# Optimization experiments

Hardware: AMD Instinct MI355X
Metric: run time of the kernel (lower is better)

## Reference

```python
import jax, jax.numpy as jnp
import numpy as np
from jax import lax

B_, S_, IN_, HID_ = 64, 512, 1024, 1024


def setup_inputs() -> dict:
    key = jax.random.key(0)
    k1, k2, k3, k4 = jax.random.split(key, 4)
    stdv = 1.0 / np.sqrt(HID_)
    return {
        "x": jax.random.normal(k1, (B_, S_, IN_), dtype=jnp.float32),
        "U": jax.random.uniform(k2, (IN_, 4 * HID_), minval=-stdv, maxval=stdv, dtype=jnp.float32),
        "V": jax.random.uniform(k3, (HID_, 4 * HID_), minval=-stdv, maxval=stdv, dtype=jnp.float32),
        "B": jax.random.uniform(k4, (4 * HID_,), minval=-stdv, maxval=stdv, dtype=jnp.float32),
        "h0": jnp.zeros((B_, HID_), dtype=jnp.float32),
        "c0": jnp.zeros((B_, HID_), dtype=jnp.float32),
    }


def reference(x, U, V, B, h0, c0):
    hd = h0.shape[-1]

    def step(carry, x_t):
        h, c = carry
        # [batch, 4*hid] combined gate pre-activation
        g = x_t @ U + h @ V + B
        n = jnp.tanh(g[:, 0:hd])                      # candidate (N_T)
        i = jax.nn.sigmoid(g[:, hd:2 * hd])           # input gate (I_T)
        f = jax.nn.sigmoid(g[:, 2 * hd:3 * hd])       # forget gate (F_T)
        o = jax.nn.sigmoid(g[:, 3 * hd:4 * hd])       # output gate (O_T)
        c_new = c * f + n * i                          # R_T
        h_new = jnp.tanh(c_new) * o                    # U_T
        return (h_new, c_new), h_new

    (h_fin, c_fin), ys = lax.scan(step, (h0, c0), jnp.swapaxes(x, 0, 1))
    out = jnp.swapaxes(ys, 0, 1)  # [batch, seq, hid]
    return out, (h_fin, c_fin)
```

## Files before the change

### kernel.cpp

```cpp
#include <hip/hip_runtime.h>
#include <stdint.h>


#define OUT_HF  33554432
#define OUT_CF  33619968

typedef __attribute__((ext_vector_type(8))) short bf16x8;
typedef __attribute__((ext_vector_type(4))) float f32x4;
typedef __attribute__((ext_vector_type(4))) unsigned short u16x4;
typedef __attribute__((ext_vector_type(4))) unsigned int u32x4;

#define WS_G    0
#define WS_XB   268435456
#define WS_HB   268435456
#define WS_UT   335544320

__device__ __forceinline__ unsigned short f2bf(float f) {
  unsigned u = __float_as_uint(f);
  u += 0x7FFFu + ((u >> 16) & 1u);
  return (unsigned short)(u >> 16);
}
__device__ __forceinline__ float bf2f(unsigned short b) {
  return __uint_as_float(((unsigned)b) << 16);
}
__device__ __forceinline__ float sigf(float x)   { return 1.0f / (1.0f + __expf(-x)); }
__device__ __forceinline__ float tanhf_(float x) { return 2.0f / (1.0f + __expf(-2.0f * x)) - 1.0f; }

__global__ void convert_x(const float* __restrict__ x, unsigned short* __restrict__ xb) {
  const int i = (blockIdx.x * 256 + threadIdx.x) * 4;
  f32x4 v = *(const f32x4*)(x + i);
  u16x4 o;
  o[0] = f2bf(v[0]); o[1] = f2bf(v[1]); o[2] = f2bf(v[2]); o[3] = f2bf(v[3]);
  *(u16x4*)(xb + i) = o;
}

__global__ void transpose_u(const float* __restrict__ U, unsigned short* __restrict__ ut) {
  __shared__ unsigned short t[64 * 65];
  const int kt = blockIdx.x;
  const int nt = blockIdx.y;
  const int tid = threadIdx.x;
  const int nn = tid & 63, kq = tid >> 6;
  #pragma unroll
  for (int i = 0; i < 16; ++i) {
    const int kk = kq * 16 + i;
    t[kk * 65 + nn] = f2bf(U[(size_t)(kt * 64 + kk) * 4096 + nt * 64 + nn]);
  }
  __syncthreads();
  const int kk2 = tid & 63, nq = tid >> 6;
  #pragma unroll
  for (int i = 0; i < 16; ++i) {
    const int nn2 = nq * 16 + i;
    ut[(size_t)(nt * 64 + nn2) * 1024 + kt * 64 + kk2] = t[kk2 * 65 + nn2];
  }
}

__global__ void init_h(const float* __restrict__ h0, uint32_t* __restrict__ hb32) {
  const int i = blockIdx.x * 256 + threadIdx.x;
  const uint32_t w0 = ((uint32_t)f2bf(h0[i])) << 16;
  const uint32_t w1 = 0xFFFFFFFFu;
  const uint32_t* p0 = hb32 + i;
  const uint32_t* p1 = hb32 + 65536 + i;
  asm volatile("global_store_dword %0, %2, off sc0 sc1\n\t"
               "global_store_dword %1, %3, off sc0 sc1"
               :: "v"(p0), "v"(p1), "v"(w0), "v"(w1) : "memory");
}

__global__ void __launch_bounds__(256) gemm_xu(const unsigned short* __restrict__ A,
                                               const unsigned short* __restrict__ Bt,
                                               unsigned short* __restrict__ Gb) {
  __shared__ __align__(16) short As[4096];
  __shared__ __align__(16) short Bs[4096];
  const int tid = threadIdx.x;
  const int l = tid & 63, w = tid >> 6;
  const int wm = w & 1, wn = w >> 1;
  const int lm = l & 15, lq = l >> 4;
  const int bid = blockIdx.x;
  const int bm = bid & 255, bn = bid >> 8;

  const int i0 = tid >> 2, kc0 = tid & 3;
  const int la0 = (kc0 * 128 + (i0 ^ (kc0 << 2))) * 8;
  const int la1 = la0 + 512;
  const unsigned short* Ap = A  + (size_t)(bm * 128 + i0) * 1024 + kc0 * 8;
  const unsigned short* Bp = Bt + (size_t)(bn * 128 + i0) * 1024 + kc0 * 8;

  f32x4 acc[4][4] = {};

  for (int kt = 0; kt < 32; ++kt) {
    const int k0 = kt * 32;
    bf16x8 av0 = *(const bf16x8*)(Ap + k0);
    bf16x8 av1 = *(const bf16x8*)(Ap + 64 * 1024 + k0);
    bf16x8 bv0 = *(const bf16x8*)(Bp + k0);
    bf16x8 bv1 = *(const bf16x8*)(Bp + 64 * 1024 + k0);
    __syncthreads();
    *(bf16x8*)(As + la0) = av0;
    *(bf16x8*)(As + la1) = av1;
    *(bf16x8*)(Bs + la0) = bv0;
    *(bf16x8*)(Bs + la1) = bv1;
    __syncthreads();

    bf16x8 af[4], bfv[4];
    #pragma unroll
    for (int mt = 0; mt < 4; ++mt) {
      const int i = wm * 64 + mt * 16 + lm;
      af[mt] = *(const bf16x8*)(As + (lq * 128 + (i ^ (lq << 2))) * 8);
    }
    #pragma unroll
    for (int nt = 0; nt < 4; ++nt) {
      const int i = wn * 64 + nt * 16 + lm;
      bfv[nt] = *(const bf16x8*)(Bs + (lq * 128 + (i ^ (lq << 2))) * 8);
    }
    #pragma unroll
    for (int mt = 0; mt < 4; ++mt)
      #pragma unroll
      for (int nt = 0; nt < 4; ++nt)
        acc[mt][nt] = __builtin_amdgcn_mfma_f32_16x16x32_bf16(af[mt], bfv[nt], acc[mt][nt], 0, 0, 0);
  }

  #pragma unroll
  for (int mt = 0; mt < 4; ++mt)
    #pragma unroll
    for (int nt = 0; nt < 4; ++nt) {
      const int col = bn * 128 + wn * 64 + nt * 16 + lm;
      const int r0  = bm * 128 + wm * 64 + mt * 16 + lq * 4;
      #pragma unroll
      for (int r = 0; r < 4; ++r)
        Gb[(size_t)(r0 + r) * 4096 + col] = f2bf(acc[mt][nt][r]);
    }
}

__global__ void __launch_bounds__(256, 1) lstm_rec(
    const unsigned short* __restrict__ Gb,
    const float* __restrict__ V,
    const float* __restrict__ Bias,
    const float* __restrict__ c0,
    uint32_t* __restrict__ hb32,
    float* __restrict__ out) {
  __shared__ __align__(16) float gbuf[4096];
  const int tid = threadIdx.x;
  const int l = tid & 63, w = tid >> 6;
  const int lm = l & 15, lq = l >> 4;
  const int bid = blockIdx.x;
  const int mb = bid & 3;
  const int nh = bid >> 2;
  const int jh = nh << 4;

  bf16x8 vf[8][4];
  {
    const int col0 = jh + lm;
    #pragma unroll
    for (int ks = 0; ks < 8; ++ks) {
      const int kb = (w << 8) + (ks << 5) + (lq << 3);
      #pragma unroll
      for (int g = 0; g < 4; ++g) {
        const size_t base = (size_t)kb * 4096 + (g << 10) + col0;
        bf16x8 v;
        #pragma unroll
        for (int jj = 0; jj < 8; ++jj)
          v[jj] = (short)f2bf(V[base + (size_t)jj * 4096]);
        vf[ks][g] = v;
      }
    }
  }

  const int b  = tid >> 4;
  const int j  = tid & 15;
  const int gr = (mb << 4) + b;
  float bias_r[4];
  #pragma unroll
  for (int g = 0; g < 4; ++g) bias_r[g] = Bias[(g << 10) + jh + j];
  float c = c0[(gr << 10) + jh + j];

  const int abase32 = ((mb << 4) + lm) * 1024 + (w << 8) + (lq << 3);

  float gp[4], gn[4];
  {
    const size_t grow = (size_t)(gr << 9) * 4096;
    #pragma unroll
    for (int g = 0; g < 4; ++g) gp[g] = bf2f(Gb[grow + (g << 10) + jh + j]);
  }

  int budget = 20000000;

  for (int t = 0; t < 512; ++t) {
    {
      const int t2 = t < 511 ? t + 1 : t;
      const size_t grow = ((size_t)(gr << 9) + t2) * 4096;
      #pragma unroll
      for (int g = 0; g < 4; ++g) gn[g] = bf2f(Gb[grow + (g << 10) + jh + j]);
    }

    const uint32_t texp = (uint32_t)t;
    const uint32_t* hp = hb32 + ((t & 1) << 16) + abase32;
    u32x4 q0, q1, q2, q3, q4, q5, q6, q7, q8, q9, q10, q11, q12, q13, q14, q15;
    do {
      asm volatile(
          "global_load_dwordx4 %0, %16, off sc0 sc1\n\t"
          "global_load_dwordx4 %1, %16, off offset:16 sc0 sc1\n\t"
          "global_load_dwordx4 %2, %16, off offset:128 sc0 sc1\n\t"
          "global_load_dwordx4 %3, %16, off offset:144 sc0 sc1\n\t"
          "global_load_dwordx4 %4, %16, off offset:256 sc0 sc1\n\t"
          "global_load_dwordx4 %5, %16, off offset:272 sc0 sc1\n\t"
          "global_load_dwordx4 %6, %16, off offset:384 sc0 sc1\n\t"
          "global_load_dwordx4 %7, %16, off offset:400 sc0 sc1\n\t"
          "global_load_dwordx4 %8, %16, off offset:512 sc0 sc1\n\t"
          "global_load_dwordx4 %9, %16, off offset:528 sc0 sc1\n\t"
          "global_load_dwordx4 %10, %16, off offset:640 sc0 sc1\n\t"
          "global_load_dwordx4 %11, %16, off offset:656 sc0 sc1\n\t"
          "global_load_dwordx4 %12, %16, off offset:768 sc0 sc1\n\t"
          "global_load_dwordx4 %13, %16, off offset:784 sc0 sc1\n\t"
          "global_load_dwordx4 %14, %16, off offset:896 sc0 sc1\n\t"
          "global_load_dwordx4 %15, %16, off offset:912 sc0 sc1\n\t"
          "s_waitcnt vmcnt(0)"
          : "=&v"(q0), "=&v"(q1), "=&v"(q2), "=&v"(q3),
            "=&v"(q4), "=&v"(q5), "=&v"(q6), "=&v"(q7),
            "=&v"(q8), "=&v"(q9), "=&v"(q10), "=&v"(q11),
            "=&v"(q12), "=&v"(q13), "=&v"(q14), "=&v"(q15)
          : "v"(hp)
          : "memory");
      #define TC4(Q) ((Q[0] ^ texp) | (Q[1] ^ texp) | (Q[2] ^ texp) | (Q[3] ^ texp))
      const uint32_t dd = TC4(q0) | TC4(q1) | TC4(q2) | TC4(q3) |
                          TC4(q4) | TC4(q5) | TC4(q6) | TC4(q7) |
                          TC4(q8) | TC4(q9) | TC4(q10) | TC4(q11) |
                          TC4(q12) | TC4(q13) | TC4(q14) | TC4(q15);
      #undef TC4
      const int stale = (dd & 0xFFFFu) != 0;
      if (!__any(stale)) break;
      __builtin_amdgcn_s_sleep(2);
    } while (--budget > 0);

    bf16x8 a[8];
    #define MK(A, QA, QB) { u32x4 pa;                                     \
      pa[0] = __builtin_amdgcn_perm(QA[1], QA[0], 0x07060302u);           \
      pa[1] = __builtin_amdgcn_perm(QA[3], QA[2], 0x07060302u);           \
      pa[2] = __builtin_amdgcn_perm(QB[1], QB[0], 0x07060302u);           \
      pa[3] = __builtin_amdgcn_perm(QB[3], QB[2], 0x07060302u);           \
      A = __builtin_bit_cast(bf16x8, pa); }
    MK(a[0], q0, q1)  MK(a[1], q2, q3)  MK(a[2], q4, q5)  MK(a[3], q6, q7)
    MK(a[4], q8, q9)  MK(a[5], q10, q11) MK(a[6], q12, q13) MK(a[7], q14, q15)
    #undef MK

    f32x4 acc[4] = {};
    #pragma unroll
    for (int ks = 0; ks < 8; ++ks)
      #pragma unroll
      for (int g = 0; g < 4; ++g)
        acc[g] = __builtin_amdgcn_mfma_f32_16x16x32_bf16(a[ks], vf[ks][g], acc[g], 0, 0, 0);

    #pragma unroll
    for (int g = 0; g < 4; ++g)
      #pragma unroll
      for (int r = 0; r < 4; ++r)
        gbuf[((w << 8) + ((lq << 2) + r) * 16 + lm) * 4 + g] = acc[g][r];

    __syncthreads();

    f32x4 hv = *(const f32x4*)(gbuf + (tid << 2));
    hv += *(const f32x4*)(gbuf + ((256 + tid) << 2));
    hv += *(const f32x4*)(gbuf + ((512 + tid) << 2));
    hv += *(const f32x4*)(gbuf + ((768 + tid) << 2));

    const float pn = hv[0] + gp[0] + bias_r[0];
    const float pi = hv[1] + gp[1] + bias_r[1];
    const float pf = hv[2] + gp[2] + bias_r[2];
    const float po = hv[3] + gp[3] + bias_r[3];
    const float nn = tanhf_(pn);
    const float ii = sigf(pi);
    const float ff = sigf(pf);
    const float oo = sigf(po);
    c = c * ff + nn * ii;
    const float h = tanhf_(c) * oo;

    out[(size_t)gr * 524288 + ((size_t)t << 10) + jh + j] = h;

    {
      const uint32_t* sp = hb32 + (((t + 1) & 1) << 16) + (gr << 10) + jh + j;
      const uint32_t hw = (((uint32_t)f2bf(h)) << 16) | ((uint32_t)(t + 1) & 0xFFFFu);
      asm volatile("global_store_dword %0, %1, off sc0 sc1"
                   :: "v"(sp), "v"(hw) : "memory");
    }

    if (t == 511) {
      out[OUT_HF + (gr << 10) + jh + j] = h;
      out[OUT_CF + (gr << 10) + jh + j] = c;
    }
    #pragma unroll
    for (int g = 0; g < 4; ++g) gp[g] = gn[g];

    __syncthreads();
  }
}

extern "C" void kernel_launch(void* const* d_in, const int* in_sizes, int n_in,
                              void* d_out, int out_size, void* d_ws, size_t ws_size,
                              hipStream_t stream) {
  const float* x  = (const float*)d_in[0];
  const float* U  = (const float*)d_in[1];
  const float* V  = (const float*)d_in[2];
  const float* Bi = (const float*)d_in[3];
  const float* h0 = (const float*)d_in[4];
  const float* c0 = (const float*)d_in[5];
  float* out = (float*)d_out;
  char* ws = (char*)d_ws;

  unsigned short* Gb = (unsigned short*)(ws + WS_G);
  unsigned short* xb = (unsigned short*)(ws + WS_XB);
  unsigned short* ut = (unsigned short*)(ws + WS_UT);
  uint32_t* hb32     = (uint32_t*)(ws + WS_HB);

  convert_x  <<<32768, 256, 0, stream>>>(x, xb);
  transpose_u<<<dim3(16, 64), 256, 0, stream>>>(U, ut);
  gemm_xu    <<<8192, 256, 0, stream>>>(xb, ut, Gb);
  init_h     <<<256, 256, 0, stream>>>(h0, hb32);
  lstm_rec   <<<256, 256, 0, stream>>>(Gb, V, Bi, c0, hb32, out);
}
```

Measured before the change: 2.998 ms.

## Add per-block step flags to gate polling of h exchange buffer

Adds a flag array where each recurrence block publishes its completed timestep after a waitcnt and barrier. Before loading h, each wave first polls the 64 flags of the blocks it depends on with a single dword load per lane and short sleeps. This replaces repeated 16-wide polling of the tagged h data. The per-step out store is moved after the flag publish so it stays off the critical path. In exchange it adds an extra barrier, a full vmcnt drain and an additional global round-trip per step, which may lengthen the serial dependency chain.

```diff
diff --git a/kernel.cpp b/kernel.cpp
--- a/kernel.cpp
+++ b/kernel.cpp
@@ -13,6 +13,7 @@
 #define WS_G    0
 #define WS_XB   268435456
 #define WS_HB   268435456
+#define WS_FL   268959744
 #define WS_UT   335544320
 
 __device__ __forceinline__ unsigned short f2bf(float f) {
@@ -54,7 +55,8 @@
   }
 }
 
-__global__ void init_h(const float* __restrict__ h0, uint32_t* __restrict__ hb32) {
+__global__ void init_h(const float* __restrict__ h0, uint32_t* __restrict__ hb32,
+                       uint32_t* __restrict__ flags) {
   const int i = blockIdx.x * 256 + threadIdx.x;
   const uint32_t w0 = ((uint32_t)f2bf(h0[i])) << 16;
   const uint32_t w1 = 0xFFFFFFFFu;
@@ -63,6 +65,12 @@
   asm volatile("global_store_dword %0, %2, off sc0 sc1\n\t"
                "global_store_dword %1, %3, off sc0 sc1"
                :: "v"(p0), "v"(p1), "v"(w0), "v"(w1) : "memory");
+  if (i < 4096) {
+    const uint32_t* fp = flags + i;
+    const uint32_t z = 0u;
+    asm volatile("global_store_dword %0, %1, off sc0 sc1"
+                 :: "v"(fp), "v"(z) : "memory");
+  }
 }
 
 __global__ void __launch_bounds__(256) gemm_xu(const unsigned short* __restrict__ A,
@@ -134,6 +142,7 @@
     const float* __restrict__ Bias,
     const float* __restrict__ c0,
     uint32_t* __restrict__ hb32,
+    uint32_t* __restrict__ flags,
     float* __restrict__ out) {
   __shared__ __align__(16) float gbuf[4096];
   const int tid = threadIdx.x;
@@ -171,6 +180,8 @@
   float c = c0[(gr << 10) + jh + j];
 
   const int abase32 = ((mb << 4) + lm) * 1024 + (w << 8) + (lq << 3);
+  const uint32_t* fwatch = flags + (((mb << 6) + l) << 4);
+  const uint32_t* fmine  = flags + (((mb << 6) + nh) << 4);
 
   float gp[4], gn[4];
   {
@@ -190,6 +201,18 @@
     }
 
     const uint32_t texp = (uint32_t)t;
+
+    {
+      uint32_t fv;
+      do {
+        asm volatile("global_load_dword %0, %1, off sc0 sc1\n\t"
+                     "s_waitcnt vmcnt(0)"
+                     : "=v"(fv) : "v"(fwatch) : "memory");
+        if (__all(fv >= texp)) break;
+        __builtin_amdgcn_s_sleep(2);
+      } while (--budget > 0);
+    }
+
     const uint32_t* hp = hb32 + ((t & 1) << 16) + abase32;
     u32x4 q0, q1, q2, q3, q4, q5, q6, q7, q8, q9, q10, q11, q12, q13, q14, q15;
     do {
@@ -270,8 +293,6 @@
     c = c * ff + nn * ii;
     const float h = tanhf_(c) * oo;
 
-    out[(size_t)gr * 524288 + ((size_t)t << 10) + jh + j] = h;
-
     {
       const uint32_t* sp = hb32 + (((t + 1) & 1) << 16) + (gr << 10) + jh + j;
       const uint32_t hw = (((uint32_t)f2bf(h)) << 16) | ((uint32_t)(t + 1) & 0xFFFFu);
@@ -279,14 +300,21 @@
                    :: "v"(sp), "v"(hw) : "memory");
     }
 
+    asm volatile("s_waitcnt vmcnt(0)" ::: "memory");
+    __syncthreads();
+    if (tid == 0) {
+      const uint32_t fw = (uint32_t)(t + 1);
+      asm volatile("global_store_dword %0, %1, off sc0 sc1"
+                   :: "v"(fmine), "v"(fw) : "memory");
+    }
+
+    out[(size_t)gr * 524288 + ((size_t)t << 10) + jh + j] = h;
     if (t == 511) {
       out[OUT_HF + (gr << 10) + jh + j] = h;
       out[OUT_CF + (gr << 10) + jh + j] = c;
     }
     #pragma unroll
     for (int g = 0; g < 4; ++g) gp[g] = gn[g];
-
-    __syncthreads();
   }
 }
 
@@ -306,10 +334,11 @@
   unsigned short* xb = (unsigned short*)(ws + WS_XB);
   unsigned short* ut = (unsigned short*)(ws + WS_UT);
   uint32_t* hb32     = (uint32_t*)(ws + WS_HB);
+  uint32_t* flg      = (uint32_t*)(ws + WS_FL);
 
   convert_x  <<<32768, 256, 0, stream>>>(x, xb);
   transpose_u<<<dim3(16, 64), 256, 0, stream>>>(U, ut);
   gemm_xu    <<<8192, 256, 0, stream>>>(xb, ut, Gb);
-  init_h     <<<256, 256, 0, stream>>>(h0, hb32);
-  lstm_rec   <<<256, 256, 0, stream>>>(Gb, V, Bi, c0, hb32, out);
-}
+  init_h     <<<256, 256, 0, stream>>>(h0, hb32, flg);
+  lstm_rec   <<<256, 256, 0, stream>>>(Gb, V, Bi, c0, hb32, flg, out);
+}
```

New measurement: 2.877 ms. -4.1%, faster.

## Add lightweight flag polling before h loads and replace syncthreads with raw barriers

Applied to the files above, without the earlier changes.

Before loading the full 16-dword h tile, each wave polls a small sample of timestamped h words (8 dwords per lane, covering its own rows and one strided set of producer columns) and spins with s_sleep until all are current. It then issues the heavy vector loads. This is meant to cut the cost of repeatedly reloading the whole h slice while other blocks are still writing it. The __syncthreads calls become raw s_barrier with sched_barrier fences, plus an explicit lgkmcnt wait before the first one. The h handoff store is moved ahead of the output store to shorten the critical path. The existing validation loop on the full tile presumably still runs afterward, so the polling adds latency on every step when the data is already ready.

```diff
diff --git a/kernel.cpp b/kernel.cpp
--- a/kernel.cpp
+++ b/kernel.cpp
@@ -143,6 +143,7 @@
   const int mb = bid & 3;
   const int nh = bid >> 2;
   const int jh = nh << 4;
+  const int wstar = nh >> 4;
 
   bf16x8 vf[8][4];
   {
@@ -171,6 +172,8 @@
   float c = c0[(gr << 10) + jh + j];
 
   const int abase32 = ((mb << 4) + lm) * 1024 + (w << 8) + (lq << 3);
+  const int poll_r = (((mb << 4) + lm) << 10) + (((w << 4) + (lq << 2)) << 4);
+  const int poll_o = (((mb << 4) + (wstar << 2) + lq) << 10) + (lm << 6);
 
   float gp[4], gn[4];
   {
@@ -190,7 +193,36 @@
     }
 
     const uint32_t texp = (uint32_t)t;
-    const uint32_t* hp = hb32 + ((t & 1) << 16) + abase32;
+    const uint32_t* bufb = hb32 + ((t & 1) << 16);
+
+    {
+      const uint32_t* pr = bufb + poll_r;
+      const uint32_t* po = bufb + poll_o;
+      uint32_t r0, r1, r2, r3, o0, o1, o2, o3;
+      do {
+        asm volatile(
+            "global_load_dword %0, %8, off sc0 sc1\n\t"
+            "global_load_dword %1, %8, off offset:64 sc0 sc1\n\t"
+            "global_load_dword %2, %8, off offset:128 sc0 sc1\n\t"
+            "global_load_dword %3, %8, off offset:192 sc0 sc1\n\t"
+            "global_load_dword %4, %9, off sc0 sc1\n\t"
+            "global_load_dword %5, %9, off offset:64 sc0 sc1\n\t"
+            "global_load_dword %6, %9, off offset:128 sc0 sc1\n\t"
+            "global_load_dword %7, %9, off offset:192 sc0 sc1\n\t"
+            "s_waitcnt vmcnt(0)"
+            : "=&v"(r0), "=&v"(r1), "=&v"(r2), "=&v"(r3),
+              "=&v"(o0), "=&v"(o1), "=&v"(o2), "=&v"(o3)
+            : "v"(pr), "v"(po)
+            : "memory");
+        const uint32_t dd = (r0 ^ texp) | (r1 ^ texp) | (r2 ^ texp) | (r3 ^ texp) |
+                            (o0 ^ texp) | (o1 ^ texp) | (o2 ^ texp) | (o3 ^ texp);
+        const int stale = (dd & 0xFFFFu) != 0;
+        if (!__any(stale)) break;
+        __builtin_amdgcn_s_sleep(2);
+      } while (--budget > 0);
+    }
+
+    const uint32_t* hp = bufb + abase32;
     u32x4 q0, q1, q2, q3, q4, q5, q6, q7, q8, q9, q10, q11, q12, q13, q14, q15;
     do {
       asm volatile(
@@ -252,7 +284,10 @@
       for (int r = 0; r < 4; ++r)
         gbuf[((w << 8) + ((lq << 2) + r) * 16 + lm) * 4 + g] = acc[g][r];
 
-    __syncthreads();
+    asm volatile("s_waitcnt lgkmcnt(0)" ::: "memory");
+    __builtin_amdgcn_sched_barrier(0);
+    __builtin_amdgcn_s_barrier();
+    __builtin_amdgcn_sched_barrier(0);
 
     f32x4 hv = *(const f32x4*)(gbuf + (tid << 2));
     hv += *(const f32x4*)(gbuf + ((256 + tid) << 2));
@@ -270,8 +305,6 @@
     c = c * ff + nn * ii;
     const float h = tanhf_(c) * oo;
 
-    out[(size_t)gr * 524288 + ((size_t)t << 10) + jh + j] = h;
-
     {
       const uint32_t* sp = hb32 + (((t + 1) & 1) << 16) + (gr << 10) + jh + j;
       const uint32_t hw = (((uint32_t)f2bf(h)) << 16) | ((uint32_t)(t + 1) & 0xFFFFu);
@@ -279,6 +312,7 @@
                    :: "v"(sp), "v"(hw) : "memory");
     }
 
+    out[(size_t)gr * 524288 + ((size_t)t << 10) + jh + j] = h;
     if (t == 511) {
       out[OUT_HF + (gr << 10) + jh + j] = h;
       out[OUT_CF + (gr << 10) + jh + j] = c;
@@ -286,7 +320,9 @@
     #pragma unroll
     for (int g = 0; g < 4; ++g) gp[g] = gn[g];
 
-    __syncthreads();
+    __builtin_amdgcn_sched_barrier(0);
+    __builtin_amdgcn_s_barrier();
+    __builtin_amdgcn_sched_barrier(0);
   }
 }
 
```

Measured after the change: 3.943 ms. 31.5% more time.
